# Kernel tuning notes

Measured on AMD Instinct MI355X. Metric: run time of the kernel, lower is better.

Reference implementation:

```python
import jax, jax.numpy as jnp
import numpy as np
from jax import lax

C = 16  # channels

def _conv1x1(x, w, b):
    # 1x1x1 Conv3d == channel-mixing einsum. x: [B,C,T,H,W], w: [O,C], b: [O]
    return jnp.einsum('oc,bcthw->bothw', w, x) + b[None, :, None, None, None]

def _ffn(x, w1, b1, w2, b2):
    return _conv1x1(jnp.tanh(_conv1x1(x, w1, b1)), w2, b2)

def setup_inputs() -> dict:
    key = jax.random.key(0)
    ks = jax.random.split(key, 12)
    s = 0.1
    x = jax.random.normal(ks[0], (2, C, 31, 256, 256), dtype=jnp.float32)
    mk_w = lambda k: jax.random.normal(k, (C, C), dtype=jnp.float32) * s
    mk_b = lambda k: jax.random.normal(k, (C,), dtype=jnp.float32) * s
    return {
        'x': x,
        'wf1': mk_w(ks[1]), 'bf1': mk_b(ks[2]),
        'wf2': mk_w(ks[3]), 'bf2': mk_b(ks[4]),
        'ww1': mk_w(ks[5]), 'bw1': mk_b(ks[6]),
        'ww2': mk_w(ks[7]), 'bw2': mk_b(ks[8]),
        'wsca': mk_w(ks[9]), 'bsca': mk_b(ks[10]),
    }

def reference(x, wf1, bf1, wf2, bf2, ww1, bw1, ww2, bw2, wsca, bsca):
    # Gates from two 1x1-conv FFNs
    Z = jnp.tanh(_ffn(x, wf1, bf1, wf2, bf2))          # [B,C,T,H,W]
    Fg = jax.nn.sigmoid(_ffn(x, ww1, bw1, ww2, bw2))   # [B,C,T,H,W]
    # Linear recurrence over time dim: h_t = f_t * h_{t-1} + (1-f_t) * z_t, h_{-1}=0
    Zt = jnp.moveaxis(Z, 2, 0)   # [T,B,C,H,W]
    Ft = jnp.moveaxis(Fg, 2, 0)
    def step(h, zf):
        z, f = zf
        h = f * h + (1.0 - f) * z
        return h, h
    h0 = jnp.zeros_like(Zt[0])
    _, hs = lax.scan(step, h0, (Zt, Ft))
    out = jnp.moveaxis(hs, 0, 2)  # [B,C,T,H,W]
    # Simplified channel attention: global avg pool -> 1x1 conv -> sigmoid -> scale
    gap = jnp.mean(out, axis=(2, 3, 4), keepdims=True)  # [B,C,1,1,1]
    att = jax.nn.sigmoid(_conv1x1(gap, wsca, bsca))
    return att * out
```

## Files before the change

kernel.cpp:

```cpp
#include <hip/hip_runtime.h>
#include <hip/hip_bf16.h>

#define TDIM 31
#define TS   65536
#define CS   (TDIM * TS)
#define BS   (16 * CS)
#define NTOT (2 * BS)
#define GAP_INV (1.0f / (31.0f * 65536.0f))

typedef __attribute__((ext_vector_type(8))) unsigned short ushort8v;
typedef float __attribute__((ext_vector_type(2))) f32x2;
typedef short __attribute__((ext_vector_type(2))) short2v;

__device__ __forceinline__ float frcp(float v){ return __builtin_amdgcn_rcpf(v); }
__device__ __forceinline__ float fexp2_(float v){ return __builtin_amdgcn_exp2f(v); }
__device__ __forceinline__ float ftanh(float x){ float e = fexp2_(x*2.8853900817779268f); return 1.0f - 2.0f*frcp(e+1.0f); }
__device__ __forceinline__ float fsigm(float x){ float e = fexp2_(x*-1.4426950408889634f); return frcp(1.0f+e); }
__device__ __forceinline__ unsigned rhu16(float x){ return (__float_as_uint(x) + 0x8000u) >> 16; }
__device__ __forceinline__ float bf2f(unsigned b){ return __uint_as_float(b << 16); }

__device__ __forceinline__ unsigned packzf(float f, float z){
#if __has_builtin(__builtin_amdgcn_cvt_pknorm_i16)
    const short2v p = __builtin_amdgcn_cvt_pknorm_i16(f, z);
    return __builtin_bit_cast(unsigned, p);
#else
    const int zi = (int)__builtin_rintf(z * 32767.0f);
    const int fi = (int)__builtin_rintf(f * 32767.0f);
    return ((unsigned)zi << 16) | ((unsigned)fi & 0xFFFFu);
#endif
}

__global__ __launch_bounds__(256) void kA_gates(
    const float* __restrict__ x,
    const float* __restrict__ wf1, const float* __restrict__ bf1,
    const float* __restrict__ wf2, const float* __restrict__ bf2,
    const float* __restrict__ ww1, const float* __restrict__ bw1,
    const float* __restrict__ ww2, const float* __restrict__ bw2,
    unsigned int* __restrict__ gates)
{
    const int tid = threadIdx.x;
    const int pos = blockIdx.x * 256 + tid;
    const int t   = blockIdx.y;
    const int b   = blockIdx.z;
    const unsigned base = (unsigned)b * BS + (unsigned)t * TS + (unsigned)pos;

    f32x2 xv2[8];
#pragma unroll
    for (int q = 0; q < 8; ++q) {
        xv2[q].x = x[base + (unsigned)(2*q)   * CS];
        xv2[q].y = x[base + (unsigned)(2*q+1) * CS];
    }

    f32x2 af2[8], aw2[8];
#pragma unroll
    for (int op = 0; op < 8; ++op) {
        const int o0 = 2 * op, o1 = 2 * op + 1;
        f32x2 a1e = {bf1[o0], 0.f}, a1o = {bf1[o1], 0.f};
        f32x2 a2e = {bw1[o0], 0.f}, a2o = {bw1[o1], 0.f};
#pragma unroll
        for (int q = 0; q < 8; ++q) {
            a1e = __builtin_elementwise_fma(*(const f32x2*)&wf1[o0*16 + q*2], xv2[q], a1e);
            a1o = __builtin_elementwise_fma(*(const f32x2*)&wf1[o1*16 + q*2], xv2[q], a1o);
            a2e = __builtin_elementwise_fma(*(const f32x2*)&ww1[o0*16 + q*2], xv2[q], a2e);
            a2o = __builtin_elementwise_fma(*(const f32x2*)&ww1[o1*16 + q*2], xv2[q], a2o);
        }
        af2[op].x = ftanh(a1e.x + a1e.y);
        af2[op].y = ftanh(a1o.x + a1o.y);
        aw2[op].x = ftanh(a2e.x + a2e.y);
        aw2[op].y = ftanh(a2o.x + a2o.y);
    }
#pragma unroll
    for (int op = 0; op < 8; ++op) {
        const int o0 = 2 * op, o1 = 2 * op + 1;
        f32x2 a1e = {bf2[o0], 0.f}, a1o = {bf2[o1], 0.f};
        f32x2 a2e = {bw2[o0], 0.f}, a2o = {bw2[o1], 0.f};
#pragma unroll
        for (int q = 0; q < 8; ++q) {
            a1e = __builtin_elementwise_fma(*(const f32x2*)&wf2[o0*16 + q*2], af2[q], a1e);
            a1o = __builtin_elementwise_fma(*(const f32x2*)&wf2[o1*16 + q*2], af2[q], a1o);
            a2e = __builtin_elementwise_fma(*(const f32x2*)&ww2[o0*16 + q*2], aw2[q], a2e);
            a2o = __builtin_elementwise_fma(*(const f32x2*)&ww2[o1*16 + q*2], aw2[q], a2o);
        }
        const float z0 = ftanh(a1e.x + a1e.y), z1 = ftanh(a1o.x + a1o.y);
        const float f0 = fsigm(a2e.x + a2e.y), f1 = fsigm(a2o.x + a2o.y);
        gates[base + (unsigned)o0 * CS] = packzf(f0, z0);
        gates[base + (unsigned)o1 * CS] = packzf(f1, z1);
    }
}

template<bool BF16H>
__global__ __launch_bounds__(256) void kB_scan(
    unsigned int* __restrict__ gates,
    unsigned short* __restrict__ hb,
    float* __restrict__ partials)
{
    const int pos = blockIdx.x * 256 + threadIdx.x;
    const int c   = blockIdx.y;
    const int b   = blockIdx.z;
    const unsigned base = (unsigned)b * BS + (unsigned)c * CS + (unsigned)pos;

    float h = 0.f, s = 0.f;
#pragma unroll
    for (int t = 0; t < TDIM; ++t) {
        const int wd = (int)gates[base + (unsigned)t * TS];
        const float z = (float)(wd >> 16) * (1.0f / 32767.0f);
        const float f = (float)((wd << 16) >> 16) * (1.0f / 32767.0f);
        h = fmaf(f, h - z, z);
        s += h;
        if (BF16H) hb[base + (unsigned)t * TS] = (unsigned short)rhu16(h);
        else       ((float*)gates)[base + (unsigned)t * TS] = h;
    }
#pragma unroll
    for (int off = 32; off; off >>= 1) s += __shfl_down(s, off, 64);
    const int lane = threadIdx.x & 63, wv = threadIdx.x >> 6;
    if (lane == 0)
        partials[(unsigned)(b * 16 + c) * 1024 + blockIdx.x * 4 + wv] = s;
}

__global__ __launch_bounds__(1024) void k2_attention(
    const float* __restrict__ partials, const float* __restrict__ wsca,
    const float* __restrict__ bsca, float* __restrict__ att)
{
    __shared__ float red[32][32];
    __shared__ float gap[32];
    const int tid = threadIdx.x;
    {
        const int bc = tid >> 5, seg = tid & 31;
        float s = 0.f;
        const float* p = partials + (unsigned)bc * 1024 + seg * 32;
#pragma unroll
        for (int j = 0; j < 32; ++j) s += p[j];
        red[bc][seg] = s;
    }
    __syncthreads();
    if (tid < 32) {
        float s = 0.f;
#pragma unroll
        for (int g = 0; g < 32; ++g) s += red[tid][g];
        gap[tid] = s * GAP_INV;
    }
    __syncthreads();
    if (tid < 32) {
        const int b = tid >> 4, o = tid & 15;
        float acc = bsca[o];
#pragma unroll
        for (int c = 0; c < 16; ++c) acc = fmaf(wsca[o*16 + c], gap[b*16 + c], acc);
        att[b*16 + o] = fsigm(acc);
    }
}

__global__ __launch_bounds__(1024) void k3_scale_b(
    const unsigned short* __restrict__ hb, const float* __restrict__ att,
    float* __restrict__ out)
{
    const int bc = blockIdx.y;
    const float a = att[bc];
    const unsigned i = blockIdx.x * 1024 + threadIdx.x;
    const size_t base = (size_t)bc * CS;
    const ushort8v v = ((const ushort8v*)(hb + base))[i];
    float4 o1, o2;
    o1.x = bf2f(v[0])*a; o1.y = bf2f(v[1])*a; o1.z = bf2f(v[2])*a; o1.w = bf2f(v[3])*a;
    o2.x = bf2f(v[4])*a; o2.y = bf2f(v[5])*a; o2.z = bf2f(v[6])*a; o2.w = bf2f(v[7])*a;
    float4* op = (float4*)(out + base);
    op[i*2]     = o1;
    op[i*2 + 1] = o2;
}

__global__ __launch_bounds__(1024) void k3_scale_a(
    const float* __restrict__ att, float* __restrict__ out)
{
    const int bc = blockIdx.y;
    const float a = att[bc];
    const unsigned i = blockIdx.x * 1024 + threadIdx.x;
    float4* op = (float4*)(out + (size_t)bc * CS);
    float4 v1 = op[i*2], v2 = op[i*2 + 1];
    v1.x *= a; v1.y *= a; v1.z *= a; v1.w *= a;
    v2.x *= a; v2.y *= a; v2.z *= a; v2.w *= a;
    op[i*2] = v1; op[i*2 + 1] = v2;
}

extern "C" void kernel_launch(void* const* d_in, const int* in_sizes, int n_in,
                              void* d_out, int out_size, void* d_ws, size_t ws_size,
                              hipStream_t stream) {
    const float* x    = (const float*)d_in[0];
    const float* wf1  = (const float*)d_in[1];
    const float* bf1  = (const float*)d_in[2];
    const float* wf2  = (const float*)d_in[3];
    const float* bf2  = (const float*)d_in[4];
    const float* ww1  = (const float*)d_in[5];
    const float* bw1  = (const float*)d_in[6];
    const float* ww2  = (const float*)d_in[7];
    const float* bw2  = (const float*)d_in[8];
    const float* wsca = (const float*)d_in[9];
    const float* bsca = (const float*)d_in[10];
    float* out = (float*)d_out;

    const size_t hbBytes   = (size_t)NTOT * 2;
    const size_t partBytes = (size_t)32 * 1024 * 4;
    const bool bf16h = ws_size >= hbBytes + partBytes + 256;

    unsigned int* gates = (unsigned int*)d_out;
    unsigned short* hb = (unsigned short*)d_ws;
    float* partials = bf16h ? (float*)((char*)d_ws + hbBytes) : (float*)d_ws;
    float* att = partials + 32 * 1024;

    kA_gates<<<dim3(256, TDIM, 2), 256, 0, stream>>>(
        x, wf1, bf1, wf2, bf2, ww1, bw1, ww2, bw2, gates);

    if (bf16h) {
        kB_scan<true><<<dim3(256, 16, 2), 256, 0, stream>>>(gates, hb, partials);
        k2_attention<<<1, 1024, 0, stream>>>(partials, wsca, bsca, att);
        k3_scale_b<<<dim3(248, 32), 1024, 0, stream>>>(hb, att, out);
    } else {
        kB_scan<false><<<dim3(256, 16, 2), 256, 0, stream>>>(gates, hb, partials);
        k2_attention<<<1, 1024, 0, stream>>>(partials, wsca, bsca, att);
        k3_scale_a<<<dim3(248, 32), 1024, 0, stream>>>(att, out);
    }
}
```

Measured before the change: 297.5 us.

## Fuse gate computation and time scan via shared-memory gate tile

Merges the gate kernel and the scan kernel into one. Each block computes packed gates for 16 spatial positions across all 31 timesteps into an XOR-swizzled LDS tile, then scans over time from LDS. This removes the global round trip of the packed gate tensor and one kernel launch. In exchange, global accesses shrink to 16-float (64-byte) segments per row, the scan loop is not unrolled, and attention now reduces 8192 partials per channel.

```diff
diff --git a/kernel.cpp b/kernel.cpp
--- a/kernel.cpp
+++ b/kernel.cpp
@@ -30,121 +30,129 @@
 #endif
 }
 
-__global__ __launch_bounds__(256) void kA_gates(
+template<bool BF16H>
+__global__ __launch_bounds__(256) void kF_fused(
     const float* __restrict__ x,
     const float* __restrict__ wf1, const float* __restrict__ bf1,
     const float* __restrict__ wf2, const float* __restrict__ bf2,
     const float* __restrict__ ww1, const float* __restrict__ bw1,
     const float* __restrict__ ww2, const float* __restrict__ bw2,
-    unsigned int* __restrict__ gates)
-{
+    float* __restrict__ out, unsigned short* __restrict__ hb,
+    float* __restrict__ partials)
+{
+    __shared__ unsigned int sGate[TDIM][16][16];
+
     const int tid = threadIdx.x;
-    const int pos = blockIdx.x * 256 + tid;
-    const int t   = blockIdx.y;
-    const int b   = blockIdx.z;
-    const unsigned base = (unsigned)b * BS + (unsigned)t * TS + (unsigned)pos;
-
-    f32x2 xv2[8];
-#pragma unroll
-    for (int q = 0; q < 8; ++q) {
-        xv2[q].x = x[base + (unsigned)(2*q)   * CS];
-        xv2[q].y = x[base + (unsigned)(2*q+1) * CS];
-    }
-
-    f32x2 af2[8], aw2[8];
-#pragma unroll
-    for (int op = 0; op < 8; ++op) {
-        const int o0 = 2 * op, o1 = 2 * op + 1;
-        f32x2 a1e = {bf1[o0], 0.f}, a1o = {bf1[o1], 0.f};
-        f32x2 a2e = {bw1[o0], 0.f}, a2o = {bw1[o1], 0.f};
-#pragma unroll
-        for (int q = 0; q < 8; ++q) {
-            a1e = __builtin_elementwise_fma(*(const f32x2*)&wf1[o0*16 + q*2], xv2[q], a1e);
-            a1o = __builtin_elementwise_fma(*(const f32x2*)&wf1[o1*16 + q*2], xv2[q], a1o);
-            a2e = __builtin_elementwise_fma(*(const f32x2*)&ww1[o0*16 + q*2], xv2[q], a2e);
-            a2o = __builtin_elementwise_fma(*(const f32x2*)&ww1[o1*16 + q*2], xv2[q], a2o);
+    const int blk = blockIdx.x;
+    const int b   = blk >> 12;
+    const int p0  = (blk & 4095) << 4;
+
+    {
+        const int t   = tid >> 4;
+        const int pos = tid & 15;
+
+        auto process = [&](int u) {
+            const unsigned base = (unsigned)b * BS + (unsigned)u * TS
+                                + (unsigned)(p0 + pos);
+            f32x2 xv2[8];
+#pragma unroll
+            for (int q = 0; q < 8; ++q) {
+                xv2[q].x = x[base + (unsigned)(2*q)   * CS];
+                xv2[q].y = x[base + (unsigned)(2*q+1) * CS];
+            }
+            const int csw = ((u & 1) << 3);
+
+            f32x2 af2[8], aw2[8];
+#pragma unroll
+            for (int op = 0; op < 8; ++op) {
+                const int o0 = 2 * op, o1 = 2 * op + 1;
+                f32x2 a1e = {bf1[o0], 0.f}, a1o = {bf1[o1], 0.f};
+                f32x2 a2e = {bw1[o0], 0.f}, a2o = {bw1[o1], 0.f};
+#pragma unroll
+                for (int q = 0; q < 8; ++q) {
+                    a1e = __builtin_elementwise_fma(*(const f32x2*)&wf1[o0*16 + q*2], xv2[q], a1e);
+                    a1o = __builtin_elementwise_fma(*(const f32x2*)&wf1[o1*16 + q*2], xv2[q], a1o);
+                    a2e = __builtin_elementwise_fma(*(const f32x2*)&ww1[o0*16 + q*2], xv2[q], a2e);
+                    a2o = __builtin_elementwise_fma(*(const f32x2*)&ww1[o1*16 + q*2], xv2[q], a2o);
+                }
+                af2[op].x = ftanh(a1e.x + a1e.y);
+                af2[op].y = ftanh(a1o.x + a1o.y);
+                aw2[op].x = ftanh(a2e.x + a2e.y);
+                aw2[op].y = ftanh(a2o.x + a2o.y);
+            }
+#pragma unroll
+            for (int op = 0; op < 8; ++op) {
+                const int o0 = 2 * op, o1 = 2 * op + 1;
+                f32x2 a1e = {bf2[o0], 0.f}, a1o = {bf2[o1], 0.f};
+                f32x2 a2e = {bw2[o0], 0.f}, a2o = {bw2[o1], 0.f};
+#pragma unroll
+                for (int q = 0; q < 8; ++q) {
+                    a1e = __builtin_elementwise_fma(*(const f32x2*)&wf2[o0*16 + q*2], af2[q], a1e);
+                    a1o = __builtin_elementwise_fma(*(const f32x2*)&wf2[o1*16 + q*2], af2[q], a1o);
+                    a2e = __builtin_elementwise_fma(*(const f32x2*)&ww2[o0*16 + q*2], aw2[q], a2e);
+                    a2o = __builtin_elementwise_fma(*(const f32x2*)&ww2[o1*16 + q*2], aw2[q], a2o);
+                }
+                const float z0 = ftanh(a1e.x + a1e.y), z1 = ftanh(a1o.x + a1o.y);
+                const float f0 = fsigm(a2e.x + a2e.y), f1 = fsigm(a2o.x + a2o.y);
+                sGate[u][o0 ^ csw][pos] = packzf(f0, z0);
+                sGate[u][o1 ^ csw][pos] = packzf(f1, z1);
+            }
+        };
+
+        process(t);
+        if (t + 16 < TDIM) process(t + 16);
+    }
+    __syncthreads();
+
+    {
+        const int c   = tid >> 4, pos = tid & 15;
+        const unsigned obase = (unsigned)b * BS + (unsigned)c * CS
+                             + (unsigned)(p0 + pos);
+        float h = 0.f, s = 0.f;
+#pragma unroll 1
+        for (int t = 0; t < TDIM; ++t) {
+            const int wd = (int)sGate[t][c ^ ((t & 1) << 3)][pos];
+            const float z = (float)(wd >> 16) * (1.0f / 32767.0f);
+            const float f = (float)((wd << 16) >> 16) * (1.0f / 32767.0f);
+            h = fmaf(f, h - z, z);
+            s += h;
+            if (BF16H) hb[obase + (unsigned)t * TS] = (unsigned short)rhu16(h);
+            else       out[obase + (unsigned)t * TS] = h;
         }
-        af2[op].x = ftanh(a1e.x + a1e.y);
-        af2[op].y = ftanh(a1o.x + a1o.y);
-        aw2[op].x = ftanh(a2e.x + a2e.y);
-        aw2[op].y = ftanh(a2o.x + a2o.y);
-    }
-#pragma unroll
-    for (int op = 0; op < 8; ++op) {
-        const int o0 = 2 * op, o1 = 2 * op + 1;
-        f32x2 a1e = {bf2[o0], 0.f}, a1o = {bf2[o1], 0.f};
-        f32x2 a2e = {bw2[o0], 0.f}, a2o = {bw2[o1], 0.f};
-#pragma unroll
-        for (int q = 0; q < 8; ++q) {
-            a1e = __builtin_elementwise_fma(*(const f32x2*)&wf2[o0*16 + q*2], af2[q], a1e);
-            a1o = __builtin_elementwise_fma(*(const f32x2*)&wf2[o1*16 + q*2], af2[q], a1o);
-            a2e = __builtin_elementwise_fma(*(const f32x2*)&ww2[o0*16 + q*2], aw2[q], a2e);
-            a2o = __builtin_elementwise_fma(*(const f32x2*)&ww2[o1*16 + q*2], aw2[q], a2o);
-        }
-        const float z0 = ftanh(a1e.x + a1e.y), z1 = ftanh(a1o.x + a1o.y);
-        const float f0 = fsigm(a2e.x + a2e.y), f1 = fsigm(a2o.x + a2o.y);
-        gates[base + (unsigned)o0 * CS] = packzf(f0, z0);
-        gates[base + (unsigned)o1 * CS] = packzf(f1, z1);
-    }
-}
-
-template<bool BF16H>
-__global__ __launch_bounds__(256) void kB_scan(
-    unsigned int* __restrict__ gates,
-    unsigned short* __restrict__ hb,
-    float* __restrict__ partials)
-{
-    const int pos = blockIdx.x * 256 + threadIdx.x;
-    const int c   = blockIdx.y;
-    const int b   = blockIdx.z;
-    const unsigned base = (unsigned)b * BS + (unsigned)c * CS + (unsigned)pos;
-
-    float h = 0.f, s = 0.f;
-#pragma unroll
-    for (int t = 0; t < TDIM; ++t) {
-        const int wd = (int)gates[base + (unsigned)t * TS];
-        const float z = (float)(wd >> 16) * (1.0f / 32767.0f);
-        const float f = (float)((wd << 16) >> 16) * (1.0f / 32767.0f);
-        h = fmaf(f, h - z, z);
-        s += h;
-        if (BF16H) hb[base + (unsigned)t * TS] = (unsigned short)rhu16(h);
-        else       ((float*)gates)[base + (unsigned)t * TS] = h;
-    }
-#pragma unroll
-    for (int off = 32; off; off >>= 1) s += __shfl_down(s, off, 64);
-    const int lane = threadIdx.x & 63, wv = threadIdx.x >> 6;
-    if (lane == 0)
-        partials[(unsigned)(b * 16 + c) * 1024 + blockIdx.x * 4 + wv] = s;
+#pragma unroll
+        for (int off = 8; off; off >>= 1) s += __shfl_down(s, off, 16);
+        if (pos == 0) partials[blk * 16 + c] = s;
+    }
 }
 
 __global__ __launch_bounds__(1024) void k2_attention(
     const float* __restrict__ partials, const float* __restrict__ wsca,
     const float* __restrict__ bsca, float* __restrict__ att)
 {
-    __shared__ float red[32][32];
-    __shared__ float gap[32];
+    __shared__ float red[2][16][32];
+    __shared__ float gap[2][16];
     const int tid = threadIdx.x;
     {
-        const int bc = tid >> 5, seg = tid & 31;
+        const int b = tid >> 9, c = (tid >> 5) & 15, seg = tid & 31;
         float s = 0.f;
-        const float* p = partials + (unsigned)bc * 1024 + seg * 32;
-#pragma unroll
-        for (int j = 0; j < 32; ++j) s += p[j];
-        red[bc][seg] = s;
+        const float* p = partials + (size_t)(b * 4096 + seg * 128) * 16 + c;
+        for (int j = 0; j < 128; ++j) s += p[j * 16];
+        red[b][c][seg] = s;
     }
     __syncthreads();
     if (tid < 32) {
+        const int b = tid >> 4, c = tid & 15;
         float s = 0.f;
 #pragma unroll
-        for (int g = 0; g < 32; ++g) s += red[tid][g];
-        gap[tid] = s * GAP_INV;
+        for (int g = 0; g < 32; ++g) s += red[b][c][g];
+        gap[b][c] = s * GAP_INV;
     }
     __syncthreads();
     if (tid < 32) {
         const int b = tid >> 4, o = tid & 15;
         float acc = bsca[o];
 #pragma unroll
-        for (int c = 0; c < 16; ++c) acc = fmaf(wsca[o*16 + c], gap[b*16 + c], acc);
+        for (int c = 0; c < 16; ++c) acc = fmaf(wsca[o*16 + c], gap[b][c], acc);
         att[b*16 + o] = fsigm(acc);
     }
 }
@@ -196,23 +204,21 @@
     float* out = (float*)d_out;
 
     const size_t hbBytes   = (size_t)NTOT * 2;
-    const size_t partBytes = (size_t)32 * 1024 * 4;
+    const size_t partBytes = (size_t)8192 * 16 * 4;
     const bool bf16h = ws_size >= hbBytes + partBytes + 256;
 
-    unsigned int* gates = (unsigned int*)d_out;
     unsigned short* hb = (unsigned short*)d_ws;
     float* partials = bf16h ? (float*)((char*)d_ws + hbBytes) : (float*)d_ws;
-    float* att = partials + 32 * 1024;
-
-    kA_gates<<<dim3(256, TDIM, 2), 256, 0, stream>>>(
-        x, wf1, bf1, wf2, bf2, ww1, bw1, ww2, bw2, gates);
+    float* att = partials + 8192 * 16;
 
     if (bf16h) {
-        kB_scan<true><<<dim3(256, 16, 2), 256, 0, stream>>>(gates, hb, partials);
+        kF_fused<true><<<8192, 256, 0, stream>>>(x, wf1, bf1, wf2, bf2,
+            ww1, bw1, ww2, bw2, out, hb, partials);
         k2_attention<<<1, 1024, 0, stream>>>(partials, wsca, bsca, att);
         k3_scale_b<<<dim3(248, 32), 1024, 0, stream>>>(hb, att, out);
     } else {
-        kB_scan<false><<<dim3(256, 16, 2), 256, 0, stream>>>(gates, hb, partials);
+        kF_fused<false><<<8192, 256, 0, stream>>>(x, wf1, bf1, wf2, bf2,
+            ww1, bw1, ww2, bw2, out, hb, partials);
         k2_attention<<<1, 1024, 0, stream>>>(partials, wsca, bsca, att);
         k3_scale_a<<<dim3(248, 32), 1024, 0, stream>>>(att, out);
     }
```

Result: slower. 380.0 us (+27.7%).
